# Performance work log

Hardware: AMD Instinct MI355X
Metric: run time of the kernel (lower is better)

The kernel has to match this reference:

```python
import jax, jax.numpy as jnp
import numpy as np

LEAK = 0.01
TEMP = 1.0
N_ORB = 1024
CTX = 32
N_ALPHA = 32
N_BETA = 32
B = 8192
EPS = 1e-20


def _leaky(x):
    return jnp.where(x >= 0, x, LEAK * x)


def _scorer_mlp(x, W1, b1, W2, b2, W3, b3):
    h = _leaky(x @ W1 + b1)
    h = _leaky(h @ W2 + b2)
    return h @ W3 + b3


def _gumbel_topk(logits, gumbel, k, temp):
    # successive-softmax subset relaxation (Plackett-Luce style)
    scores0 = logits + gumbel

    def step(carry, _):
        scores, khot = carry
        onehot = jax.nn.softmax(scores / temp, axis=-1)
        khot = khot + onehot
        scores = scores + jnp.log(jnp.maximum(1.0 - onehot, EPS))
        return (scores, khot), None

    (_, khot), _ = jax.lax.scan(step, (scores0, jnp.zeros_like(scores0)), None, length=k)
    return khot


def _soft_to_hard(soft, k):
    # straight-through: hard forward, soft backward
    idx = jax.lax.top_k(soft, k)[1]                      # (B, k)
    bidx = jnp.arange(soft.shape[0])[:, None]
    hard = jnp.zeros_like(soft).at[bidx, idx].set(1.0)
    return jax.lax.stop_gradient(hard - soft) + soft


def _lin_init(key, fan_in, fan_out):
    s = 1.0 / np.sqrt(fan_in)
    k1, k2 = jax.random.split(key)
    W = jax.random.uniform(k1, (fan_in, fan_out), minval=-s, maxval=s, dtype=jnp.float32)
    b = jax.random.uniform(k2, (fan_out,), minval=-s, maxval=s, dtype=jnp.float32)
    return W, b


def setup_inputs() -> dict:
    key = jax.random.key(0)
    ks = jax.random.split(key, 12)
    # alpha scorer: input = n_orb (baseline only, context_dim=0)
    W1a, b1a = _lin_init(ks[0], N_ORB, 128)
    W2a, b2a = _lin_init(ks[1], 128, 64)
    W3a, b3a = _lin_init(ks[2], 64, N_ORB)
    # beta scorer: context proj n_orb -> 32, input = n_orb + 32
    Wc, bc = _lin_init(ks[3], N_ORB, CTX)
    W1b, b1b = _lin_init(ks[4], N_ORB + CTX, 128)
    W2b, b2b = _lin_init(ks[5], 128, 64)
    W3b, b3b = _lin_init(ks[6], 64, N_ORB)
    baseline_a = jnp.zeros((N_ORB,), jnp.float32)
    baseline_b = jnp.zeros((N_ORB,), jnp.float32)
    # Gumbel noise: -log(-log(U))
    ua = jax.random.uniform(ks[7], (B, N_ORB), minval=1e-6, maxval=1.0 - 1e-6)
    ub = jax.random.uniform(ks[8], (B, N_ORB), minval=1e-6, maxval=1.0 - 1e-6)
    g_alpha = -jnp.log(-jnp.log(ua))
    g_beta = -jnp.log(-jnp.log(ub))
    return {
        "baseline_a": baseline_a, "W1a": W1a, "b1a": b1a, "W2a": W2a, "b2a": b2a,
        "W3a": W3a, "b3a": b3a,
        "baseline_b": baseline_b, "Wc": Wc, "bc": bc, "W1b": W1b, "b1b": b1b,
        "W2b": W2b, "b2b": b2b, "W3b": W3b, "b3b": b3b,
        "g_alpha": g_alpha, "g_beta": g_beta,
        "batch_size": B,
    }


def reference(baseline_a, W1a, b1a, W2a, b2a, W3a, b3a,
              baseline_b, Wc, bc, W1b, b1b, W2b, b2b, W3b, b3b,
              g_alpha, g_beta, batch_size):
    # --- alpha scoring (context_dim = 0) ---
    base_a = jnp.broadcast_to(baseline_a, (batch_size, N_ORB))
    alpha_logits = _scorer_mlp(base_a, W1a, b1a, W2a, b2a, W3a, b3a) + base_a
    alpha_soft = _gumbel_topk(alpha_logits, g_alpha, N_ALPHA, TEMP)
    alpha_config = _soft_to_hard(alpha_soft, N_ALPHA)          # (B, N_ORB)
    # --- beta scoring conditioned on alpha config ---
    base_b = jnp.broadcast_to(baseline_b, (batch_size, N_ORB))
    ctx = alpha_config @ Wc + bc                               # (B, 32)
    net_in = jnp.concatenate([base_b, ctx], axis=-1)
    beta_logits = _scorer_mlp(net_in, W1b, b1b, W2b, b2b, W3b, b3b) + base_b
    beta_soft = _gumbel_topk(beta_logits, g_beta, N_BETA, TEMP)
    beta_config = _soft_to_hard(beta_soft, N_BETA)
    return jnp.concatenate([alpha_config, beta_config], axis=-1)  # (B, num_sites)
```

## Files before the change

### kernel.cpp

```cpp
#include <hip/hip_runtime.h>
#include <hip/hip_bf16.h>
#include <float.h>

#define N_ORB 1024
#define KSEL 32
#define LEAK 0.01f
#define LOG2E 1.4426950408889634f

typedef float f32x2 __attribute__((ext_vector_type(2)));

__device__ __forceinline__ float leaky(float x) { return x >= 0.0f ? x : LEAK * x; }

template <int CTRL, int RM>
__device__ __forceinline__ int dpp0_i(int v) {
  return __builtin_amdgcn_update_dpp(0, v, CTRL, RM, 0xF, true);
}
template <int CTRL>
__device__ __forceinline__ float dpp_zero(float v) {
  return __int_as_float(
      __builtin_amdgcn_update_dpp(0, __float_as_int(v), CTRL, 0xF, 0xF, true));
}
__device__ __forceinline__ float rdlane(float v, int l) {
  return __int_as_float(__builtin_amdgcn_readlane(__float_as_int(v), l));
}

__device__ __forceinline__ float wave_sum64_dpp(float v) {
  v += dpp_zero<0x111>(v);
  v += dpp_zero<0x112>(v);
  v += dpp_zero<0x114>(v);
  v += dpp_zero<0x118>(v);
  v += dpp_zero<0x142>(v);
  v += dpp_zero<0x143>(v);
  return rdlane(v, 63);
}
__device__ __forceinline__ int wave_isum64(int v) {
  v += dpp0_i<0x111, 0xF>(v);
  v += dpp0_i<0x112, 0xF>(v);
  v += dpp0_i<0x114, 0xF>(v);
  v += dpp0_i<0x118, 0xF>(v);
  v += dpp0_i<0x142, 0xF>(v);
  v += dpp0_i<0x143, 0xF>(v);
  return __builtin_amdgcn_readlane(v, 63);
}
__device__ __forceinline__ int wave_iscan64(int v) {
  v += dpp0_i<0x111, 0xF>(v);
  v += dpp0_i<0x112, 0xF>(v);
  v += dpp0_i<0x114, 0xF>(v);
  v += dpp0_i<0x118, 0xF>(v);
  v += dpp0_i<0x142, 0xA>(v);
  v += dpp0_i<0x143, 0xC>(v);
  return v;
}

__device__ void run_chain2(f32x2 w[16], f32x2 kh[16]) {
#pragma unroll
  for (int i = 0; i < 16; ++i) kh[i] = f32x2{0.0f, 0.0f};
  const f32x2 onev = f32x2{1.0f, 1.0f};
  const f32x2 zerov = f32x2{0.0f, 0.0f};
#pragma unroll 2
  for (int it = 0; it < KSEL; ++it) {
    f32x2 t0 = w[0] + w[1], t1 = w[2] + w[3], t2 = w[4] + w[5], t3 = w[6] + w[7];
    f32x2 t4 = w[8] + w[9], t5 = w[10] + w[11], t6 = w[12] + w[13], t7 = w[14] + w[15];
    t0 += t1; t2 += t3; t4 += t5; t6 += t7;
    t0 += t2; t4 += t6;
    t0 += t4;
    float Z0 = wave_sum64_dpp(t0.x);
    float Z1 = wave_sum64_dpp(t0.y);
    Z0 = fmaxf(Z0, 1e-30f);
    Z1 = fmaxf(Z1, 1e-30f);
    float r0 = __builtin_amdgcn_rcpf(Z0);
    float r1 = __builtin_amdgcn_rcpf(Z1);
    float rZ0 = __builtin_fmaf(__builtin_fmaf(-Z0, r0, 1.0f), r0, r0);
    float rZ1 = __builtin_fmaf(__builtin_fmaf(-Z1, r1, 1.0f), r1, r1);
    const f32x2 rZ = f32x2{rZ0, rZ1};
#pragma unroll
    for (int i = 0; i < 16; ++i) {
      kh[i] = __builtin_elementwise_fma(w[i], rZ, kh[i]);
      f32x2 om = __builtin_elementwise_fma(-w[i], rZ, onev);
      om = __builtin_elementwise_min(__builtin_elementwise_max(om, zerov), onev);
      w[i] = w[i] * om;
    }
  }
}

__device__ unsigned tie_mask16(const f32x2 kh[16], bool comp_y, unsigned T,
                               int lane) {
  unsigned gt = 0, eq = 0;
#pragma unroll
  for (int i = 0; i < 16; ++i) {
    const unsigned u = __float_as_uint(comp_y ? kh[i].y : kh[i].x);
    gt |= (u > T ? 1u : 0u) << i;
    eq |= (u == T ? 1u : 0u) << i;
  }
  const int n_gt = wave_isum64(__popc(gt));
  const int m = 32 - n_gt;
  const int pe = __popc(eq);
  const int be = wave_iscan64(pe) - pe;
  int need = m - be;
  need = need < 0 ? 0 : (need > pe ? pe : need);
  unsigned tk = 0;
  unsigned em = eq;
  for (int guard = 0; guard < 16; ++guard) {
    if (!__any(need > 0)) break;
    if (need > 0) {
      const int bpos = __ffs(em) - 1;
      tk |= 1u << bpos;
      em &= em - 1;
      --need;
    }
  }
  return gt | tk;
}

__device__ void top32_mask2(const f32x2 kh[16], int lane, unsigned& m0,
                            unsigned& m1) {
  unsigned lo0 = 0, lo1 = 0;
  bool ex0 = false, ex1 = false;
  for (int b = 30; b >= 0; --b) {
    const unsigned c0v = lo0 | (1u << b);
    const unsigned c1v = lo1 | (1u << b);
    int c0 = 0, c1 = 0;
#pragma unroll
    for (int i = 0; i < 16; ++i) {
      c0 += __popcll(__ballot(__float_as_uint(kh[i].x) >= c0v));
      c1 += __popcll(__ballot(__float_as_uint(kh[i].y) >= c1v));
    }
    if (!ex0 && c0 >= 32) { lo0 = c0v; ex0 = (c0 == 32); }
    if (!ex1 && c1 >= 32) { lo1 = c1v; ex1 = (c1 == 32); }
    if (ex0 && ex1) break;
  }

  if (ex0) {
    unsigned mk = 0;
#pragma unroll
    for (int i = 0; i < 16; ++i)
      mk |= (__float_as_uint(kh[i].x) >= lo0 ? 1u : 0u) << i;
    m0 = mk;
  } else {
    m0 = tie_mask16(kh, false, lo0, lane);
  }
  if (ex1) {
    unsigned mk = 0;
#pragma unroll
    for (int i = 0; i < 16; ++i)
      mk |= (__float_as_uint(kh[i].y) >= lo1 ? 1u : 0u) << i;
    m1 = mk;
  } else {
    m1 = tie_mask16(kh, true, lo1, lane);
  }
}

__device__ __forceinline__ void compact_idx(unsigned mask, int lane,
                                            int* __restrict__ dst) {
  const int pe = __popc(mask);
  int base = wave_iscan64(pe) - pe;
  unsigned m = mask;
  while (m) {
    const int s = __ffs(m) - 1;
    m &= m - 1;
    dst[base++] = (lane << 4) | s;
  }
}

__device__ __forceinline__ void write_half(float* __restrict__ dst,
                                           unsigned mask, int lane) {
  float4* o4 = (float4*)dst;
#pragma unroll
  for (int q = 0; q < 4; ++q) {
    float4 o;
    o.x = ((mask >> (4 * q + 0)) & 1) ? 1.0f : 0.0f;
    o.y = ((mask >> (4 * q + 1)) & 1) ? 1.0f : 0.0f;
    o.z = ((mask >> (4 * q + 2)) & 1) ? 1.0f : 0.0f;
    o.w = ((mask >> (4 * q + 3)) & 1) ? 1.0f : 0.0f;
    o4[lane * 4 + q] = o;
  }
}

extern "C" __global__ void pcfs_pre1(const float* __restrict__ ba,
                                     const float* __restrict__ W1a,
                                     const float* __restrict__ b1a,
                                     const float* __restrict__ bb,
                                     const float* __restrict__ W1b,
                                     float* __restrict__ ws) {
  const int b = blockIdx.x;
  const int t = threadIdx.x;
  float acc = 0.0f;
  if (b < 128) {
#pragma unroll
    for (int j = t; j < N_ORB; j += 256) acc += ba[j] * W1a[j * 128 + b];
  } else {
    const int n = b - 128;
#pragma unroll
    for (int j = t; j < N_ORB; j += 256) acc += bb[j] * W1b[j * 128 + n];
  }
  __shared__ float red[4];
  float wsum = wave_sum64_dpp(acc);
  if ((t & 63) == 0) red[t >> 6] = wsum;
  __syncthreads();
  if (t == 0) {
    float tot = red[0] + red[1] + red[2] + red[3];
    if (b < 128)
      ws[1152 + b] = leaky(tot + b1a[b]);
    else
      ws[N_ORB + (b - 128)] = tot;
  }
}

extern "C" __global__ void pcfs_pre2(const float* __restrict__ ba,
                                     const float* __restrict__ W2a,
                                     const float* __restrict__ b2a,
                                     const float* __restrict__ W3a,
                                     const float* __restrict__ b3a,
                                     float* __restrict__ ws) {
  __shared__ float h1[128];
  __shared__ float h2[64];
  const int t = threadIdx.x;
  if (t < 128) h1[t] = ws[1152 + t];
  __syncthreads();
  if (t < 64) {
    float acc = b2a[t];
#pragma unroll 8
    for (int n = 0; n < 128; ++n) acc += h1[n] * W2a[n * 64 + t];
    h2[t] = leaky(acc);
  }
  __syncthreads();
  float acc = b3a[t];
#pragma unroll 8
  for (int m = 0; m < 64; ++m) acc += h2[m] * W3a[m * N_ORB + t];
  ws[t] = acc + ba[t];
}

extern "C" __global__ void __launch_bounds__(256)
    __attribute__((amdgpu_waves_per_eu(4, 4))) pcfs_sampler(
    const float* __restrict__ ws, const float* __restrict__ Wc,
    const float* __restrict__ bc, const float* __restrict__ W1b,
    const float* __restrict__ b1b, const float* __restrict__ W2b,
    const float* __restrict__ b2b, const float* __restrict__ W3b,
    const float* __restrict__ b3b, const float* __restrict__ bb,
    const float* __restrict__ g_alpha, const float* __restrict__ g_beta,
    float* __restrict__ out, int B) {
  __shared__ int sidx[4][64];
  const int wave = threadIdx.x >> 6;
  const int lane = threadIdx.x & 63;
  const int pair = blockIdx.x * 4 + wave;
  const int row0 = pair * 2;
  if (row0 >= B) return;
  const bool have1 = (row0 + 1 < B);
  const int row1 = have1 ? row0 + 1 : row0;

  f32x2 w[16], kh[16];

  {
    const float4* c4 = (const float4*)ws;
    const float4* g40 = (const float4*)(g_alpha + (size_t)row0 * N_ORB);
    const float4* g41 = (const float4*)(g_alpha + (size_t)row1 * N_ORB);
#pragma unroll
    for (int q = 0; q < 4; ++q) {
      float4 c = c4[lane * 4 + q];
      float4 g0 = g40[lane * 4 + q];
      float4 g1 = g41[lane * 4 + q];
      w[4 * q + 0] = f32x2{__builtin_amdgcn_exp2f((c.x + g0.x) * LOG2E),
                           __builtin_amdgcn_exp2f((c.x + g1.x) * LOG2E)};
      w[4 * q + 1] = f32x2{__builtin_amdgcn_exp2f((c.y + g0.y) * LOG2E),
                           __builtin_amdgcn_exp2f((c.y + g1.y) * LOG2E)};
      w[4 * q + 2] = f32x2{__builtin_amdgcn_exp2f((c.z + g0.z) * LOG2E),
                           __builtin_amdgcn_exp2f((c.z + g1.z) * LOG2E)};
      w[4 * q + 3] = f32x2{__builtin_amdgcn_exp2f((c.w + g0.w) * LOG2E),
                           __builtin_amdgcn_exp2f((c.w + g1.w) * LOG2E)};
    }
  }
  run_chain2(w, kh);
  unsigned am0, am1;
  top32_mask2(kh, lane, am0, am1);

  write_half(out + (size_t)row0 * (2 * N_ORB), am0, lane);
  if (have1) write_half(out + (size_t)row1 * (2 * N_ORB), am1, lane);

  compact_idx(am0, lane, &sidx[wave][0]);
  compact_idx(am1, lane, &sidx[wave][32]);
  const int vi0 = sidx[wave][lane & 31];
  const int vi1 = sidx[wave][32 + (lane & 31)];
  const float bcv = bc[lane & 31];
  float ctx0 = bcv, ctx1 = bcv;
#pragma unroll
  for (int r = 0; r < 32; ++r) {
    const int i0 = __builtin_amdgcn_readlane(vi0, r);
    const int i1 = __builtin_amdgcn_readlane(vi1, r);
    ctx0 += Wc[i0 * 32 + (lane & 31)];
    ctx1 += Wc[i1 * 32 + (lane & 31)];
  }

  f32x2 h1a, h1b_;
  {
    const float ia = b1b[lane] + ws[N_ORB + lane];
    const float ib = b1b[lane + 64] + ws[N_ORB + lane + 64];
    h1a = f32x2{ia, ia};
    h1b_ = f32x2{ib, ib};
  }
#pragma unroll 4
  for (int c = 0; c < 32; ++c) {
    const f32x2 cv = f32x2{rdlane(ctx0, c), rdlane(ctx1, c)};
    const float* wr = W1b + (size_t)(N_ORB + c) * 128;
    const float wa = wr[lane], wb = wr[lane + 64];
    h1a = __builtin_elementwise_fma(f32x2{wa, wa}, cv, h1a);
    h1b_ = __builtin_elementwise_fma(f32x2{wb, wb}, cv, h1b_);
  }
  h1a = f32x2{leaky(h1a.x), leaky(h1a.y)};
  h1b_ = f32x2{leaky(h1b_.x), leaky(h1b_.y)};

  f32x2 h2p0, h2p1, h2p2, h2p3;
  {
    const float i2 = b2b[lane];
    h2p0 = f32x2{i2, i2};
    h2p1 = f32x2{0.0f, 0.0f};
    h2p2 = f32x2{0.0f, 0.0f};
    h2p3 = f32x2{0.0f, 0.0f};
  }
#pragma unroll 4
  for (int n = 0; n < 64; n += 4) {
    const f32x2 v0 = f32x2{rdlane(h1a.x, n + 0), rdlane(h1a.y, n + 0)};
    const f32x2 v1 = f32x2{rdlane(h1a.x, n + 1), rdlane(h1a.y, n + 1)};
    const f32x2 v2 = f32x2{rdlane(h1a.x, n + 2), rdlane(h1a.y, n + 2)};
    const f32x2 v3 = f32x2{rdlane(h1a.x, n + 3), rdlane(h1a.y, n + 3)};
    const float w0 = W2b[(n + 0) * 64 + lane];
    const float w1 = W2b[(n + 1) * 64 + lane];
    const float w2 = W2b[(n + 2) * 64 + lane];
    const float w3 = W2b[(n + 3) * 64 + lane];
    h2p0 = __builtin_elementwise_fma(f32x2{w0, w0}, v0, h2p0);
    h2p1 = __builtin_elementwise_fma(f32x2{w1, w1}, v1, h2p1);
    h2p2 = __builtin_elementwise_fma(f32x2{w2, w2}, v2, h2p2);
    h2p3 = __builtin_elementwise_fma(f32x2{w3, w3}, v3, h2p3);
  }
#pragma unroll 4
  for (int n = 0; n < 64; n += 4) {
    const f32x2 v0 = f32x2{rdlane(h1b_.x, n + 0), rdlane(h1b_.y, n + 0)};
    const f32x2 v1 = f32x2{rdlane(h1b_.x, n + 1), rdlane(h1b_.y, n + 1)};
    const f32x2 v2 = f32x2{rdlane(h1b_.x, n + 2), rdlane(h1b_.y, n + 2)};
    const f32x2 v3 = f32x2{rdlane(h1b_.x, n + 3), rdlane(h1b_.y, n + 3)};
    const float w0 = W2b[(n + 64 + 0) * 64 + lane];
    const float w1 = W2b[(n + 64 + 1) * 64 + lane];
    const float w2 = W2b[(n + 64 + 2) * 64 + lane];
    const float w3 = W2b[(n + 64 + 3) * 64 + lane];
    h2p0 = __builtin_elementwise_fma(f32x2{w0, w0}, v0, h2p0);
    h2p1 = __builtin_elementwise_fma(f32x2{w1, w1}, v1, h2p1);
    h2p2 = __builtin_elementwise_fma(f32x2{w2, w2}, v2, h2p2);
    h2p3 = __builtin_elementwise_fma(f32x2{w3, w3}, v3, h2p3);
  }
  f32x2 h2v = (h2p0 + h2p1) + (h2p2 + h2p3);
  h2v = f32x2{leaky(h2v.x), leaky(h2v.y)};

  {
    const float4* b4 = (const float4*)b3b;
#pragma unroll
    for (int q = 0; q < 4; ++q) {
      float4 b = b4[lane * 4 + q];
      w[4 * q + 0] = f32x2{b.x, b.x};
      w[4 * q + 1] = f32x2{b.y, b.y};
      w[4 * q + 2] = f32x2{b.z, b.z};
      w[4 * q + 3] = f32x2{b.w, b.w};
    }
  }
#pragma unroll 4
  for (int m = 0; m < 64; ++m) {
    const f32x2 hm = f32x2{rdlane(h2v.x, m), rdlane(h2v.y, m)};
    const float4* w4 = (const float4*)(W3b + m * N_ORB);
#pragma unroll
    for (int q = 0; q < 4; ++q) {
      float4 wv = w4[lane * 4 + q];
      w[4 * q + 0] = __builtin_elementwise_fma(f32x2{wv.x, wv.x}, hm, w[4 * q + 0]);
      w[4 * q + 1] = __builtin_elementwise_fma(f32x2{wv.y, wv.y}, hm, w[4 * q + 1]);
      w[4 * q + 2] = __builtin_elementwise_fma(f32x2{wv.z, wv.z}, hm, w[4 * q + 2]);
      w[4 * q + 3] = __builtin_elementwise_fma(f32x2{wv.w, wv.w}, hm, w[4 * q + 3]);
    }
  }
  {
    const float4* bb4 = (const float4*)bb;
    const float4* g40 = (const float4*)(g_beta + (size_t)row0 * N_ORB);
    const float4* g41 = (const float4*)(g_beta + (size_t)row1 * N_ORB);
#pragma unroll
    for (int q = 0; q < 4; ++q) {
      float4 b = bb4[lane * 4 + q];
      const float4 g0 = g40[lane * 4 + q];
      const float4 g1 = g41[lane * 4 + q];
      w[4 * q + 0] = f32x2{
          __builtin_amdgcn_exp2f((w[4 * q + 0].x + b.x + g0.x) * LOG2E),
          __builtin_amdgcn_exp2f((w[4 * q + 0].y + b.x + g1.x) * LOG2E)};
      w[4 * q + 1] = f32x2{
          __builtin_amdgcn_exp2f((w[4 * q + 1].x + b.y + g0.y) * LOG2E),
          __builtin_amdgcn_exp2f((w[4 * q + 1].y + b.y + g1.y) * LOG2E)};
      w[4 * q + 2] = f32x2{
          __builtin_amdgcn_exp2f((w[4 * q + 2].x + b.z + g0.z) * LOG2E),
          __builtin_amdgcn_exp2f((w[4 * q + 2].y + b.z + g1.z) * LOG2E)};
      w[4 * q + 3] = f32x2{
          __builtin_amdgcn_exp2f((w[4 * q + 3].x + b.w + g0.w) * LOG2E),
          __builtin_amdgcn_exp2f((w[4 * q + 3].y + b.w + g1.w) * LOG2E)};
    }
  }
  run_chain2(w, kh);
  unsigned bm0, bm1;
  top32_mask2(kh, lane, bm0, bm1);

  write_half(out + (size_t)row0 * (2 * N_ORB) + N_ORB, bm0, lane);
  if (have1) write_half(out + (size_t)row1 * (2 * N_ORB) + N_ORB, bm1, lane);
}

extern "C" void kernel_launch(void* const* d_in, const int* in_sizes, int n_in,
                              void* d_out, int out_size, void* d_ws, size_t ws_size,
                              hipStream_t stream) {
  const float* ba  = (const float*)d_in[0];
  const float* W1a = (const float*)d_in[1];
  const float* b1a = (const float*)d_in[2];
  const float* W2a = (const float*)d_in[3];
  const float* b2a = (const float*)d_in[4];
  const float* W3a = (const float*)d_in[5];
  const float* b3a = (const float*)d_in[6];
  const float* bb  = (const float*)d_in[7];
  const float* Wc  = (const float*)d_in[8];
  const float* bc  = (const float*)d_in[9];
  const float* W1b = (const float*)d_in[10];
  const float* b1b = (const float*)d_in[11];
  const float* W2b = (const float*)d_in[12];
  const float* b2b = (const float*)d_in[13];
  const float* W3b = (const float*)d_in[14];
  const float* b3b = (const float*)d_in[15];
  const float* ga  = (const float*)d_in[16];
  const float* gbt = (const float*)d_in[17];
  const int B = in_sizes[16] / N_ORB;
  float* ws = (float*)d_ws;

  hipLaunchKernelGGL(pcfs_pre1, dim3(256), dim3(256), 0, stream,
                     ba, W1a, b1a, bb, W1b, ws);
  hipLaunchKernelGGL(pcfs_pre2, dim3(1), dim3(1024), 0, stream,
                     ba, W2a, b2a, W3a, b3a, ws);
  const int pairs = (B + 1) / 2;
  hipLaunchKernelGGL(pcfs_sampler, dim3((pairs + 3) / 4), dim3(256), 0, stream,
                     ws, Wc, bc, W1b, b1b, W2b, b2b, W3b, b3b, bb,
                     ga, gbt, (float*)d_out, B);
}
```

Before: 274.5 us.

## Process one row per wave instead of two packed rows to raise occupancy

The sampler kernel stops packing two batch rows per wave into float2 vectors and handles a single row per wave, with scalar chains, top-k and MLP code. The launch bound moves from 4 waves per EU to 8 blocks per CU, and the grid doubles. This lowers register pressure so more waves can hide the latency of the serial softmax chain and the weight loads. In exchange it gives up packed-FMA throughput, doubles the cross-lane reductions per row, and re-reads the shared MLP weights once per row instead of once per pair.

Result: slower. 321.9 us (+17.3%).

```diff
diff --git a/kernel.cpp b/kernel.cpp
--- a/kernel.cpp
+++ b/kernel.cpp
@@ -6,8 +6,6 @@
 #define KSEL 32
 #define LEAK 0.01f
 #define LOG2E 1.4426950408889634f
-
-typedef float f32x2 __attribute__((ext_vector_type(2)));
 
 __device__ __forceinline__ float leaky(float x) { return x >= 0.0f ? x : LEAK * x; }
 
@@ -52,43 +50,35 @@
   return v;
 }
 
-__device__ void run_chain2(f32x2 w[16], f32x2 kh[16]) {
-#pragma unroll
-  for (int i = 0; i < 16; ++i) kh[i] = f32x2{0.0f, 0.0f};
-  const f32x2 onev = f32x2{1.0f, 1.0f};
-  const f32x2 zerov = f32x2{0.0f, 0.0f};
+__device__ void run_chain1(float w[16], float kh[16]) {
+#pragma unroll
+  for (int i = 0; i < 16; ++i) kh[i] = 0.0f;
 #pragma unroll 2
   for (int it = 0; it < KSEL; ++it) {
-    f32x2 t0 = w[0] + w[1], t1 = w[2] + w[3], t2 = w[4] + w[5], t3 = w[6] + w[7];
-    f32x2 t4 = w[8] + w[9], t5 = w[10] + w[11], t6 = w[12] + w[13], t7 = w[14] + w[15];
+    float t0 = w[0] + w[1], t1 = w[2] + w[3], t2 = w[4] + w[5], t3 = w[6] + w[7];
+    float t4 = w[8] + w[9], t5 = w[10] + w[11], t6 = w[12] + w[13], t7 = w[14] + w[15];
     t0 += t1; t2 += t3; t4 += t5; t6 += t7;
     t0 += t2; t4 += t6;
     t0 += t4;
-    float Z0 = wave_sum64_dpp(t0.x);
-    float Z1 = wave_sum64_dpp(t0.y);
-    Z0 = fmaxf(Z0, 1e-30f);
-    Z1 = fmaxf(Z1, 1e-30f);
-    float r0 = __builtin_amdgcn_rcpf(Z0);
-    float r1 = __builtin_amdgcn_rcpf(Z1);
-    float rZ0 = __builtin_fmaf(__builtin_fmaf(-Z0, r0, 1.0f), r0, r0);
-    float rZ1 = __builtin_fmaf(__builtin_fmaf(-Z1, r1, 1.0f), r1, r1);
-    const f32x2 rZ = f32x2{rZ0, rZ1};
+    float Z = wave_sum64_dpp(t0);
+    Z = fmaxf(Z, 1e-30f);
+    float r = __builtin_amdgcn_rcpf(Z);
+    float rZ = __builtin_fmaf(__builtin_fmaf(-Z, r, 1.0f), r, r);
 #pragma unroll
     for (int i = 0; i < 16; ++i) {
-      kh[i] = __builtin_elementwise_fma(w[i], rZ, kh[i]);
-      f32x2 om = __builtin_elementwise_fma(-w[i], rZ, onev);
-      om = __builtin_elementwise_min(__builtin_elementwise_max(om, zerov), onev);
+      kh[i] = __builtin_fmaf(w[i], rZ, kh[i]);
+      float om = __builtin_fmaf(-w[i], rZ, 1.0f);
+      om = fminf(fmaxf(om, 0.0f), 1.0f);
       w[i] = w[i] * om;
     }
   }
 }
 
-__device__ unsigned tie_mask16(const f32x2 kh[16], bool comp_y, unsigned T,
-                               int lane) {
+__device__ unsigned tie_mask1(const float kh[16], unsigned T, int lane) {
   unsigned gt = 0, eq = 0;
 #pragma unroll
   for (int i = 0; i < 16; ++i) {
-    const unsigned u = __float_as_uint(comp_y ? kh[i].y : kh[i].x);
+    const unsigned u = __float_as_uint(kh[i]);
     gt |= (u > T ? 1u : 0u) << i;
     eq |= (u == T ? 1u : 0u) << i;
   }
@@ -112,42 +102,28 @@
   return gt | tk;
 }
 
-__device__ void top32_mask2(const f32x2 kh[16], int lane, unsigned& m0,
-                            unsigned& m1) {
-  unsigned lo0 = 0, lo1 = 0;
-  bool ex0 = false, ex1 = false;
+__device__ unsigned top32_mask1(const float kh[16], int lane) {
+  unsigned lo = 0;
+  bool ex = false;
   for (int b = 30; b >= 0; --b) {
-    const unsigned c0v = lo0 | (1u << b);
-    const unsigned c1v = lo1 | (1u << b);
-    int c0 = 0, c1 = 0;
-#pragma unroll
-    for (int i = 0; i < 16; ++i) {
-      c0 += __popcll(__ballot(__float_as_uint(kh[i].x) >= c0v));
-      c1 += __popcll(__ballot(__float_as_uint(kh[i].y) >= c1v));
-    }
-    if (!ex0 && c0 >= 32) { lo0 = c0v; ex0 = (c0 == 32); }
-    if (!ex1 && c1 >= 32) { lo1 = c1v; ex1 = (c1 == 32); }
-    if (ex0 && ex1) break;
-  }
-
-  if (ex0) {
+    const unsigned cv = lo | (1u << b);
+    int c = 0;
+#pragma unroll
+    for (int i = 0; i < 16; ++i)
+      c += __popcll(__ballot(__float_as_uint(kh[i]) >= cv));
+    if (c >= 32) {
+      lo = cv;
+      if (c == 32) { ex = true; break; }
+    }
+  }
+  if (ex) {
     unsigned mk = 0;
 #pragma unroll
     for (int i = 0; i < 16; ++i)
-      mk |= (__float_as_uint(kh[i].x) >= lo0 ? 1u : 0u) << i;
-    m0 = mk;
-  } else {
-    m0 = tie_mask16(kh, false, lo0, lane);
-  }
-  if (ex1) {
-    unsigned mk = 0;
-#pragma unroll
-    for (int i = 0; i < 16; ++i)
-      mk |= (__float_as_uint(kh[i].y) >= lo1 ? 1u : 0u) << i;
-    m1 = mk;
-  } else {
-    m1 = tie_mask16(kh, true, lo1, lane);
-  }
+      mk |= (__float_as_uint(kh[i]) >= lo ? 1u : 0u) << i;
+    return mk;
+  }
+  return tie_mask1(kh, lo, lane);
 }
 
 __device__ __forceinline__ void compact_idx(unsigned mask, int lane,
@@ -230,8 +206,7 @@
   ws[t] = acc + ba[t];
 }
 
-extern "C" __global__ void __launch_bounds__(256)
-    __attribute__((amdgpu_waves_per_eu(4, 4))) pcfs_sampler(
+extern "C" __global__ void __launch_bounds__(256, 8) pcfs_sampler(
     const float* __restrict__ ws, const float* __restrict__ Wc,
     const float* __restrict__ bc, const float* __restrict__ W1b,
     const float* __restrict__ b1b, const float* __restrict__ W2b,
@@ -239,169 +214,112 @@
     const float* __restrict__ b3b, const float* __restrict__ bb,
     const float* __restrict__ g_alpha, const float* __restrict__ g_beta,
     float* __restrict__ out, int B) {
-  __shared__ int sidx[4][64];
+  __shared__ int sidx[4][32];
   const int wave = threadIdx.x >> 6;
   const int lane = threadIdx.x & 63;
-  const int pair = blockIdx.x * 4 + wave;
-  const int row0 = pair * 2;
-  if (row0 >= B) return;
-  const bool have1 = (row0 + 1 < B);
-  const int row1 = have1 ? row0 + 1 : row0;
-
-  f32x2 w[16], kh[16];
+  const int row = blockIdx.x * 4 + wave;
+  if (row >= B) return;
+
+  float w[16], kh[16];
 
   {
     const float4* c4 = (const float4*)ws;
-    const float4* g40 = (const float4*)(g_alpha + (size_t)row0 * N_ORB);
-    const float4* g41 = (const float4*)(g_alpha + (size_t)row1 * N_ORB);
+    const float4* g4 = (const float4*)(g_alpha + (size_t)row * N_ORB);
 #pragma unroll
     for (int q = 0; q < 4; ++q) {
       float4 c = c4[lane * 4 + q];
-      float4 g0 = g40[lane * 4 + q];
-      float4 g1 = g41[lane * 4 + q];
-      w[4 * q + 0] = f32x2{__builtin_amdgcn_exp2f((c.x + g0.x) * LOG2E),
-                           __builtin_amdgcn_exp2f((c.x + g1.x) * LOG2E)};
-      w[4 * q + 1] = f32x2{__builtin_amdgcn_exp2f((c.y + g0.y) * LOG2E),
-                           __builtin_amdgcn_exp2f((c.y + g1.y) * LOG2E)};
-      w[4 * q + 2] = f32x2{__builtin_amdgcn_exp2f((c.z + g0.z) * LOG2E),
-                           __builtin_amdgcn_exp2f((c.z + g1.z) * LOG2E)};
-      w[4 * q + 3] = f32x2{__builtin_amdgcn_exp2f((c.w + g0.w) * LOG2E),
-                           __builtin_amdgcn_exp2f((c.w + g1.w) * LOG2E)};
-    }
-  }
-  run_chain2(w, kh);
-  unsigned am0, am1;
-  top32_mask2(kh, lane, am0, am1);
-
-  write_half(out + (size_t)row0 * (2 * N_ORB), am0, lane);
-  if (have1) write_half(out + (size_t)row1 * (2 * N_ORB), am1, lane);
-
-  compact_idx(am0, lane, &sidx[wave][0]);
-  compact_idx(am1, lane, &sidx[wave][32]);
-  const int vi0 = sidx[wave][lane & 31];
-  const int vi1 = sidx[wave][32 + (lane & 31)];
-  const float bcv = bc[lane & 31];
-  float ctx0 = bcv, ctx1 = bcv;
+      float4 g = g4[lane * 4 + q];
+      w[4 * q + 0] = __builtin_amdgcn_exp2f((c.x + g.x) * LOG2E);
+      w[4 * q + 1] = __builtin_amdgcn_exp2f((c.y + g.y) * LOG2E);
+      w[4 * q + 2] = __builtin_amdgcn_exp2f((c.z + g.z) * LOG2E);
+      w[4 * q + 3] = __builtin_amdgcn_exp2f((c.w + g.w) * LOG2E);
+    }
+  }
+  run_chain1(w, kh);
+  const unsigned am = top32_mask1(kh, lane);
+
+  write_half(out + (size_t)row * (2 * N_ORB), am, lane);
+
+  compact_idx(am, lane, sidx[wave]);
+  const int vi = sidx[wave][lane & 31];
+  float ctx = bc[lane & 31];
 #pragma unroll
   for (int r = 0; r < 32; ++r) {
-    const int i0 = __builtin_amdgcn_readlane(vi0, r);
-    const int i1 = __builtin_amdgcn_readlane(vi1, r);
-    ctx0 += Wc[i0 * 32 + (lane & 31)];
-    ctx1 += Wc[i1 * 32 + (lane & 31)];
-  }
-
-  f32x2 h1a, h1b_;
-  {
-    const float ia = b1b[lane] + ws[N_ORB + lane];
-    const float ib = b1b[lane + 64] + ws[N_ORB + lane + 64];
-    h1a = f32x2{ia, ia};
-    h1b_ = f32x2{ib, ib};
-  }
+    const int i0 = __builtin_amdgcn_readlane(vi, r);
+    ctx += Wc[i0 * 32 + (lane & 31)];
+  }
+
+  float h1a = b1b[lane] + ws[N_ORB + lane];
+  float h1b = b1b[lane + 64] + ws[N_ORB + lane + 64];
 #pragma unroll 4
   for (int c = 0; c < 32; ++c) {
-    const f32x2 cv = f32x2{rdlane(ctx0, c), rdlane(ctx1, c)};
+    const float cv = rdlane(ctx, c);
     const float* wr = W1b + (size_t)(N_ORB + c) * 128;
-    const float wa = wr[lane], wb = wr[lane + 64];
-    h1a = __builtin_elementwise_fma(f32x2{wa, wa}, cv, h1a);
-    h1b_ = __builtin_elementwise_fma(f32x2{wb, wb}, cv, h1b_);
-  }
-  h1a = f32x2{leaky(h1a.x), leaky(h1a.y)};
-  h1b_ = f32x2{leaky(h1b_.x), leaky(h1b_.y)};
-
-  f32x2 h2p0, h2p1, h2p2, h2p3;
-  {
-    const float i2 = b2b[lane];
-    h2p0 = f32x2{i2, i2};
-    h2p1 = f32x2{0.0f, 0.0f};
-    h2p2 = f32x2{0.0f, 0.0f};
-    h2p3 = f32x2{0.0f, 0.0f};
-  }
+    h1a = __builtin_fmaf(wr[lane], cv, h1a);
+    h1b = __builtin_fmaf(wr[lane + 64], cv, h1b);
+  }
+  h1a = leaky(h1a);
+  h1b = leaky(h1b);
+
+  float p0 = b2b[lane], p1 = 0.0f, p2 = 0.0f, p3 = 0.0f;
 #pragma unroll 4
   for (int n = 0; n < 64; n += 4) {
-    const f32x2 v0 = f32x2{rdlane(h1a.x, n + 0), rdlane(h1a.y, n + 0)};
-    const f32x2 v1 = f32x2{rdlane(h1a.x, n + 1), rdlane(h1a.y, n + 1)};
-    const f32x2 v2 = f32x2{rdlane(h1a.x, n + 2), rdlane(h1a.y, n + 2)};
-    const f32x2 v3 = f32x2{rdlane(h1a.x, n + 3), rdlane(h1a.y, n + 3)};
-    const float w0 = W2b[(n + 0) * 64 + lane];
-    const float w1 = W2b[(n + 1) * 64 + lane];
-    const float w2 = W2b[(n + 2) * 64 + lane];
-    const float w3 = W2b[(n + 3) * 64 + lane];
-    h2p0 = __builtin_elementwise_fma(f32x2{w0, w0}, v0, h2p0);
-    h2p1 = __builtin_elementwise_fma(f32x2{w1, w1}, v1, h2p1);
-    h2p2 = __builtin_elementwise_fma(f32x2{w2, w2}, v2, h2p2);
-    h2p3 = __builtin_elementwise_fma(f32x2{w3, w3}, v3, h2p3);
+    p0 = __builtin_fmaf(W2b[(n + 0) * 64 + lane], rdlane(h1a, n + 0), p0);
+    p1 = __builtin_fmaf(W2b[(n + 1) * 64 + lane], rdlane(h1a, n + 1), p1);
+    p2 = __builtin_fmaf(W2b[(n + 2) * 64 + lane], rdlane(h1a, n + 2), p2);
+    p3 = __builtin_fmaf(W2b[(n + 3) * 64 + lane], rdlane(h1a, n + 3), p3);
   }
 #pragma unroll 4
   for (int n = 0; n < 64; n += 4) {
-    const f32x2 v0 = f32x2{rdlane(h1b_.x, n + 0), rdlane(h1b_.y, n + 0)};
-    const f32x2 v1 = f32x2{rdlane(h1b_.x, n + 1), rdlane(h1b_.y, n + 1)};
-    const f32x2 v2 = f32x2{rdlane(h1b_.x, n + 2), rdlane(h1b_.y, n + 2)};
-    const f32x2 v3 = f32x2{rdlane(h1b_.x, n + 3), rdlane(h1b_.y, n + 3)};
-    const float w0 = W2b[(n + 64 + 0) * 64 + lane];
-    const float w1 = W2b[(n + 64 + 1) * 64 + lane];
-    const float w2 = W2b[(n + 64 + 2) * 64 + lane];
-    const float w3 = W2b[(n + 64 + 3) * 64 + lane];
-    h2p0 = __builtin_elementwise_fma(f32x2{w0, w0}, v0, h2p0);
-    h2p1 = __builtin_elementwise_fma(f32x2{w1, w1}, v1, h2p1);
-    h2p2 = __builtin_elementwise_fma(f32x2{w2, w2}, v2, h2p2);
-    h2p3 = __builtin_elementwise_fma(f32x2{w3, w3}, v3, h2p3);
-  }
-  f32x2 h2v = (h2p0 + h2p1) + (h2p2 + h2p3);
-  h2v = f32x2{leaky(h2v.x), leaky(h2v.y)};
+    p0 = __builtin_fmaf(W2b[(n + 64 + 0) * 64 + lane], rdlane(h1b, n + 0), p0);
+    p1 = __builtin_fmaf(W2b[(n + 64 + 1) * 64 + lane], rdlane(h1b, n + 1), p1);
+    p2 = __builtin_fmaf(W2b[(n + 64 + 2) * 64 + lane], rdlane(h1b, n + 2), p2);
+    p3 = __builtin_fmaf(W2b[(n + 64 + 3) * 64 + lane], rdlane(h1b, n + 3), p3);
+  }
+  float h2v = (p0 + p1) + (p2 + p3);
+  h2v = leaky(h2v);
 
   {
     const float4* b4 = (const float4*)b3b;
 #pragma unroll
     for (int q = 0; q < 4; ++q) {
       float4 b = b4[lane * 4 + q];
-      w[4 * q + 0] = f32x2{b.x, b.x};
-      w[4 * q + 1] = f32x2{b.y, b.y};
-      w[4 * q + 2] = f32x2{b.z, b.z};
-      w[4 * q + 3] = f32x2{b.w, b.w};
+      w[4 * q + 0] = b.x;
+      w[4 * q + 1] = b.y;
+      w[4 * q + 2] = b.z;
+      w[4 * q + 3] = b.w;
     }
   }
 #pragma unroll 4
   for (int m = 0; m < 64; ++m) {
-    const f32x2 hm = f32x2{rdlane(h2v.x, m), rdlane(h2v.y, m)};
+    const float hm = rdlane(h2v, m);
     const float4* w4 = (const float4*)(W3b + m * N_ORB);
 #pragma unroll
     for (int q = 0; q < 4; ++q) {
       float4 wv = w4[lane * 4 + q];
-      w[4 * q + 0] = __builtin_elementwise_fma(f32x2{wv.x, wv.x}, hm, w[4 * q + 0]);
-      w[4 * q + 1] = __builtin_elementwise_fma(f32x2{wv.y, wv.y}, hm, w[4 * q + 1]);
-      w[4 * q + 2] = __builtin_elementwise_fma(f32x2{wv.z, wv.z}, hm, w[4 * q + 2]);
-      w[4 * q + 3] = __builtin_elementwise_fma(f32x2{wv.w, wv.w}, hm, w[4 * q + 3]);
+      w[4 * q + 0] = __builtin_fmaf(wv.x, hm, w[4 * q + 0]);
+      w[4 * q + 1] = __builtin_fmaf(wv.y, hm, w[4 * q + 1]);
+      w[4 * q + 2] = __builtin_fmaf(wv.z, hm, w[4 * q + 2]);
+      w[4 * q + 3] = __builtin_fmaf(wv.w, hm, w[4 * q + 3]);
     }
   }
   {
     const float4* bb4 = (const float4*)bb;
-    const float4* g40 = (const float4*)(g_beta + (size_t)row0 * N_ORB);
-    const float4* g41 = (const float4*)(g_beta + (size_t)row1 * N_ORB);
+    const float4* g4 = (const float4*)(g_beta + (size_t)row * N_ORB);
 #pragma unroll
     for (int q = 0; q < 4; ++q) {
       float4 b = bb4[lane * 4 + q];
-      const float4 g0 = g40[lane * 4 + q];
-      const float4 g1 = g41[lane * 4 + q];
-      w[4 * q + 0] = f32x2{
-          __builtin_amdgcn_exp2f((w[4 * q + 0].x + b.x + g0.x) * LOG2E),
-          __builtin_amdgcn_exp2f((w[4 * q + 0].y + b.x + g1.x) * LOG2E)};
-      w[4 * q + 1] = f32x2{
-          __builtin_amdgcn_exp2f((w[4 * q + 1].x + b.y + g0.y) * LOG2E),
-          __builtin_amdgcn_exp2f((w[4 * q + 1].y + b.y + g1.y) * LOG2E)};
-      w[4 * q + 2] = f32x2{
-          __builtin_amdgcn_exp2f((w[4 * q + 2].x + b.z + g0.z) * LOG2E),
-          __builtin_amdgcn_exp2f((w[4 * q + 2].y + b.z + g1.z) * LOG2E)};
-      w[4 * q + 3] = f32x2{
-          __builtin_amdgcn_exp2f((w[4 * q + 3].x + b.w + g0.w) * LOG2E),
-          __builtin_amdgcn_exp2f((w[4 * q + 3].y + b.w + g1.w) * LOG2E)};
-    }
-  }
-  run_chain2(w, kh);
-  unsigned bm0, bm1;
-  top32_mask2(kh, lane, bm0, bm1);
-
-  write_half(out + (size_t)row0 * (2 * N_ORB) + N_ORB, bm0, lane);
-  if (have1) write_half(out + (size_t)row1 * (2 * N_ORB) + N_ORB, bm1, lane);
+      float4 g = g4[lane * 4 + q];
+      w[4 * q + 0] = __builtin_amdgcn_exp2f((w[4 * q + 0] + b.x + g.x) * LOG2E);
+      w[4 * q + 1] = __builtin_amdgcn_exp2f((w[4 * q + 1] + b.y + g.y) * LOG2E);
+      w[4 * q + 2] = __builtin_amdgcn_exp2f((w[4 * q + 2] + b.z + g.z) * LOG2E);
+      w[4 * q + 3] = __builtin_amdgcn_exp2f((w[4 * q + 3] + b.w + g.w) * LOG2E);
+    }
+  }
+  run_chain1(w, kh);
+  const unsigned bm = top32_mask1(kh, lane);
+
+  write_half(out + (size_t)row * (2 * N_ORB) + N_ORB, bm, lane);
 }
 
 extern "C" void kernel_launch(void* const* d_in, const int* in_sizes, int n_in,
@@ -432,8 +350,7 @@
                      ba, W1a, b1a, bb, W1b, ws);
   hipLaunchKernelGGL(pcfs_pre2, dim3(1), dim3(1024), 0, stream,
                      ba, W2a, b2a, W3a, b3a, ws);
-  const int pairs = (B + 1) / 2;
-  hipLaunchKernelGGL(pcfs_sampler, dim3((pairs + 3) / 4), dim3(256), 0, stream,
+  hipLaunchKernelGGL(pcfs_sampler, dim3((B + 3) / 4), dim3(256), 0, stream,
                      ws, Wc, bc, W1b, b1b, W2b, b2b, W3b, b3b, bb,
                      ga, gbt, (float*)d_out, B);
 }
```
